# Kernel optimization log

Hardware: AMD Instinct MI355X
Metric: run time of the kernel (lower is better)

The kernel has to match this reference:

```python
import jax, jax.numpy as jnp
import numpy as np

D = 1024
H = 16
HEAD_DIM = D // H

def setup_inputs() -> dict:
    key = jax.random.key(0)
    ks = jax.random.split(key, 5)
    B, T = 2, 2048
    scale = 0.02
    x = jax.random.normal(ks[0], (B, T, D), dtype=jnp.float32)
    W_kqv = jax.random.normal(ks[1], (D, 3 * D), dtype=jnp.float32) * scale
    b_kqv = jnp.zeros((3 * D,), dtype=jnp.float32)
    W_proj = jax.random.normal(ks[2], (D, D), dtype=jnp.float32) * scale
    b_proj = jnp.zeros((D,), dtype=jnp.float32)
    return {"x": x, "W_kqv": W_kqv, "b_kqv": b_kqv, "W_proj": W_proj, "b_proj": b_proj}

def reference(x, W_kqv, b_kqv, W_proj, b_proj):
    B, T, d = x.shape
    qkv = x @ W_kqv + b_kqv  # [B,T,3d]
    q, k, v = jnp.split(qkv, 3, axis=-1)
    # [B, h, T, head_dim]
    def heads(t):
        return t.reshape(B, T, H, HEAD_DIM).transpose(0, 2, 1, 3)
    q, k, v = heads(q), heads(k), heads(v)
    scores = jnp.einsum("bhqd,bhkd->bhqk", q, k) / jnp.sqrt(jnp.float32(HEAD_DIM))
    causal = jnp.tril(jnp.ones((T, T), dtype=bool))  # True = keep
    scores = jnp.where(causal[None, None], scores, -jnp.inf)
    attn = jax.nn.softmax(scores, axis=-1)
    out = jnp.einsum("bhqk,bhkd->bhqd", attn, v)
    out = out.transpose(0, 2, 1, 3).reshape(B, T, d)
    return out @ W_proj + b_proj
```

## Files before the change

kernel.cpp:

```cpp
#include <hip/hip_runtime.h>
#include <hip/hip_bf16.h>
#include <cstdint>

typedef __bf16 bf16_t;
typedef __bf16 bf16x8 __attribute__((ext_vector_type(8)));
typedef __bf16 bf16x4 __attribute__((ext_vector_type(4)));
typedef float  f32x4  __attribute__((ext_vector_type(4)));

static constexpr int Bb = 2;
static constexpr int Tt = 2048;
static constexpr int Dd = 1024;
static constexpr int Hh = 16;
static constexpr int HD = 64;

#define QSCALE 0.18033688011112042f

__device__ __forceinline__ void async_copy16(const bf16_t* gsrc, bf16_t* ldst) {
    __builtin_amdgcn_global_load_lds(
        (const __attribute__((address_space(1))) unsigned int*)gsrc,
        (__attribute__((address_space(3))) unsigned int*)ldst, 16, 0, 0);
}

__global__ __launch_bounds__(256) void cvt_bf16_kernel(const float* __restrict__ in,
                                                       bf16_t* __restrict__ out, int n) {
    int i = (blockIdx.x * 256 + threadIdx.x) * 8;
    if (i >= n) return;
    float4 v0 = *(const float4*)(in + i);
    float4 v1 = *(const float4*)(in + i + 4);
    bf16x8 o;
    o[0] = (bf16_t)v0.x; o[1] = (bf16_t)v0.y; o[2] = (bf16_t)v0.z; o[3] = (bf16_t)v0.w;
    o[4] = (bf16_t)v1.x; o[5] = (bf16_t)v1.y; o[6] = (bf16_t)v1.z; o[7] = (bf16_t)v1.w;
    *(bf16x8*)(out + i) = o;
}

__global__ __launch_bounds__(256) void transpose_cvt(const float* __restrict__ in,
                                                     bf16_t* __restrict__ out,
                                                     int R, int C) {
    __shared__ bf16_t tile[64][72];
    int tr = blockIdx.y * 64, tc = blockIdx.x * 64;
    int t = threadIdx.x;
    int r = t >> 4;
    int c4 = (t & 15) * 4;
#pragma unroll
    for (int rr = 0; rr < 4; ++rr) {
        int row = r + rr * 16;
        float4 v = *(const float4*)(in + (size_t)(tr + row) * C + tc + c4);
        tile[c4 + 0][row] = (bf16_t)v.x;
        tile[c4 + 1][row] = (bf16_t)v.y;
        tile[c4 + 2][row] = (bf16_t)v.z;
        tile[c4 + 3][row] = (bf16_t)v.w;
    }
    __syncthreads();
#pragma unroll
    for (int rr = 0; rr < 4; ++rr) {
        int oc = r + rr * 16;
        bf16x4 o;
        o[0] = tile[oc][c4 + 0];
        o[1] = tile[oc][c4 + 1];
        o[2] = tile[oc][c4 + 2];
        o[3] = tile[oc][c4 + 3];
        *(bf16x4*)(out + (size_t)(tc + oc) * R + tr + c4) = o;
    }
}

template <int MODE, int NT>
__global__ __launch_bounds__(256) void gemm_bt(
    const bf16_t* __restrict__ A, const bf16_t* __restrict__ Bt,
    const float* __restrict__ bias, float* __restrict__ Cout,
    bf16_t* __restrict__ qb_, bf16_t* __restrict__ kb_, bf16_t* __restrict__ vb_,
    int M, int N, int K) {
    constexpr int NFRAG = NT / 32;
    __shared__ bf16_t As[128 * 64];
    __shared__ bf16_t Bs[NT * 64];
    int t = threadIdx.x;
    int wave = t >> 6, lane = t & 63;
    int l15 = lane & 15, quad = lane >> 4;
    int wm = wave & 1, wn = wave >> 1;
    int m0 = blockIdx.y * 128, n0 = blockIdx.x * NT;

    f32x4 acc[4][NFRAG];
#pragma unroll
    for (int mi = 0; mi < 4; ++mi)
#pragma unroll
        for (int ni = 0; ni < NFRAG; ++ni) acc[mi][ni] = (f32x4){0.f, 0.f, 0.f, 0.f};

    int kx = l15 & 7;

    for (int kk = 0; kk < K; kk += 64) {
        __syncthreads();
#pragma unroll
        for (int j = 0; j < 4; ++j) {
            int cid = j * 256 + t;
            int row = cid >> 3, sub = (cid & 7) ^ (row & 7);
            async_copy16(A + (size_t)(m0 + row) * K + kk + sub * 8, &As[cid * 8]);
        }
#pragma unroll
        for (int j = 0; j < NT / 32; ++j) {
            int cid = j * 256 + t;
            int row = cid >> 3, sub = (cid & 7) ^ (row & 7);
            async_copy16(Bt + (size_t)(n0 + row) * K + kk + sub * 8, &Bs[cid * 8]);
        }
        __syncthreads();
#pragma unroll
        for (int kb = 0; kb < 2; ++kb) {
            bf16x8 af[4], bf[NFRAG];
#pragma unroll
            for (int mi = 0; mi < 4; ++mi) {
                int r = wm * 64 + mi * 16 + l15;
                af[mi] = *(const bf16x8*)(&As[r * 64 + ((kb * 4 + quad) ^ kx) * 8]);
            }
#pragma unroll
            for (int ni = 0; ni < NFRAG; ++ni) {
                int r = wn * (NT / 2) + ni * 16 + l15;
                bf[ni] = *(const bf16x8*)(&Bs[r * 64 + ((kb * 4 + quad) ^ kx) * 8]);
            }
#pragma unroll
            for (int mi = 0; mi < 4; ++mi)
#pragma unroll
                for (int ni = 0; ni < NFRAG; ++ni)
                    acc[mi][ni] = __builtin_amdgcn_mfma_f32_16x16x32_bf16(af[mi], bf[ni], acc[mi][ni], 0, 0, 0);
        }
    }

    if (MODE == 1 && (n0 >> 10) == 2) {
#pragma unroll
        for (int ni = 0; ni < NFRAG; ++ni) {
            int col = n0 + wn * (NT / 2) + ni * 16 + l15;
            float bv = bias[col];
            int hh = (col >> 6) & 15, dd = col & 63;
#pragma unroll
            for (int mi = 0; mi < 4; ++mi) {
                int row = m0 + wm * 64 + mi * 16 + quad * 4;
                int bb = row >> 11, tt = row & (Tt - 1);
                bf16x4 pv;
#pragma unroll
                for (int r = 0; r < 4; ++r) pv[r] = (bf16_t)(acc[mi][ni][r] + bv);
                *(bf16x4*)(vb_ + ((size_t)(bb * Hh + hh) * HD + dd) * Tt + tt) = pv;
            }
        }
        return;
    }

#pragma unroll
    for (int ni = 0; ni < NFRAG; ++ni) {
        int col = n0 + wn * (NT / 2) + ni * 16 + l15;
        float bv = bias[col];
#pragma unroll
        for (int mi = 0; mi < 4; ++mi) {
#pragma unroll
            for (int r = 0; r < 4; ++r) {
                int row = m0 + wm * 64 + mi * 16 + quad * 4 + r;
                float v = acc[mi][ni][r] + bv;
                if (MODE == 0) {
                    Cout[(size_t)row * N + col] = v;
                } else {
                    int sec = col >> 10;
                    int hh = (col >> 6) & 15, dd = col & 63;
                    int bb = row >> 11, tt = row & (Tt - 1);
                    size_t idx = (((size_t)(bb * Hh + hh)) * Tt + tt) * HD + dd;
                    if (sec == 0) qb_[idx] = (bf16_t)(v * QSCALE);
                    else          kb_[idx] = (bf16_t)v;
                }
            }
        }
    }
}

__global__ __launch_bounds__(256, 4) void attn_kernel(
    const bf16_t* __restrict__ qb, const bf16_t* __restrict__ kb,
    const bf16_t* __restrict__ vb, bf16_t* __restrict__ ab) {
    __shared__ bf16_t Ks[64][72];
    __shared__ bf16_t Vs[64][72];
    __shared__ bf16_t Ps[4][16][72];
    int t = threadIdx.x;
    int wave = t >> 6, lane = t & 63;
    int l15 = lane & 15, quad = lane >> 4;
    int bh = blockIdx.y;
    int x = blockIdx.x;
    int qt = ((bh >> 3) & 1) ? (31 - x) : x;
    int b = bh >> 4, h = bh & 15;
    int qbase = qt * 64 + wave * 16;
    int q = qbase + l15;
    const bf16_t* qptr = qb + (size_t)bh * Tt * HD;
    const bf16_t* kptr = kb + (size_t)bh * Tt * HD;
    const bf16_t* vptr = vb + (size_t)bh * HD * Tt;

    bf16x8 qf[2];
    qf[0] = *(const bf16x8*)(qptr + (size_t)q * HD + quad * 8);
    qf[1] = *(const bf16x8*)(qptr + (size_t)q * HD + 32 + quad * 8);

    f32x4 o[4];
#pragma unroll
    for (int g = 0; g < 4; ++g) o[g] = (f32x4){0.f, 0.f, 0.f, 0.f};
    float mrow = -1e30f, lrow = 0.f;

    int srow = t >> 2;
    int scol = (t & 3) * 16;
    int qmax_w = qbase + 15;

    int nkt = qt + 1;
    for (int it = 0; it < nkt; ++it) {
        int kt0 = it * 64;
        __syncthreads();
        const bf16_t* kg = kptr + (size_t)(kt0 + srow) * HD + scol;
        *(bf16x8*)(&Ks[srow][scol])     = *(const bf16x8*)(kg);
        *(bf16x8*)(&Ks[srow][scol + 8]) = *(const bf16x8*)(kg + 8);
        const bf16_t* vg = vptr + (size_t)srow * Tt + kt0 + scol;
        *(bf16x8*)(&Vs[srow][scol])     = *(const bf16x8*)(vg);
        *(bf16x8*)(&Vs[srow][scol + 8]) = *(const bf16x8*)(vg + 8);
        __syncthreads();
        if (kt0 > qmax_w) continue;

        f32x4 s[4];
#pragma unroll
        for (int g = 0; g < 4; ++g) {
            s[g] = (f32x4){0.f, 0.f, 0.f, 0.f};
            bf16x8 kf0 = *(const bf16x8*)(&Ks[g * 16 + l15][quad * 8]);
            bf16x8 kf1 = *(const bf16x8*)(&Ks[g * 16 + l15][32 + quad * 8]);
            s[g] = __builtin_amdgcn_mfma_f32_16x16x32_bf16(kf0, qf[0], s[g], 0, 0, 0);
            s[g] = __builtin_amdgcn_mfma_f32_16x16x32_bf16(kf1, qf[1], s[g], 0, 0, 0);
        }

        if (kt0 + 63 > qbase) {
#pragma unroll
            for (int g = 0; g < 4; ++g)
#pragma unroll
                for (int r = 0; r < 4; ++r) {
                    int k_abs = kt0 + g * 16 + quad * 4 + r;
                    s[g][r] = (k_abs > q) ? -1e30f : s[g][r];
                }
        }

        float mloc = -1e30f;
#pragma unroll
        for (int g = 0; g < 4; ++g)
            mloc = fmaxf(mloc, fmaxf(fmaxf(s[g][0], s[g][1]), fmaxf(s[g][2], s[g][3])));
        mloc = fmaxf(mloc, __shfl_xor(mloc, 16));
        mloc = fmaxf(mloc, __shfl_xor(mloc, 32));
        float mnew = fmaxf(mrow, mloc);
        float alpha = exp2f(mrow - mnew);
        mrow = mnew;

        float rs = 0.f;
#pragma unroll
        for (int g = 0; g < 4; ++g) {
            float p0 = exp2f(s[g][0] - mnew);
            float p1 = exp2f(s[g][1] - mnew);
            float p2 = exp2f(s[g][2] - mnew);
            float p3 = exp2f(s[g][3] - mnew);
            rs += (p0 + p1) + (p2 + p3);
            bf16x4 pk;
            pk[0] = (bf16_t)p0; pk[1] = (bf16_t)p1; pk[2] = (bf16_t)p2; pk[3] = (bf16_t)p3;
            *(bf16x4*)(&Ps[wave][l15][g * 16 + quad * 4]) = pk;
        }
        rs += __shfl_xor(rs, 16);
        rs += __shfl_xor(rs, 32);
        lrow = lrow * alpha + rs;

#pragma unroll
        for (int g = 0; g < 4; ++g)
#pragma unroll
            for (int r = 0; r < 4; ++r) o[g][r] *= alpha;

#pragma unroll
        for (int kc = 0; kc < 2; ++kc) {
            bf16x8 pf = *(const bf16x8*)(&Ps[wave][l15][kc * 32 + quad * 8]);
#pragma unroll
            for (int g = 0; g < 4; ++g) {
                bf16x8 vf = *(const bf16x8*)(&Vs[g * 16 + l15][kc * 32 + quad * 8]);
                o[g] = __builtin_amdgcn_mfma_f32_16x16x32_bf16(vf, pf, o[g], 0, 0, 0);
            }
        }
    }

    float inv = 1.0f / lrow;
    size_t obase = ((size_t)b * Tt + q) * Dd + h * 64;
#pragma unroll
    for (int g = 0; g < 4; ++g) {
        bf16x4 ov;
#pragma unroll
        for (int r = 0; r < 4; ++r) ov[r] = (bf16_t)(o[g][r] * inv);
        *(bf16x4*)(ab + obase + g * 16 + quad * 4) = ov;
    }
}

extern "C" void kernel_launch(void* const* d_in, const int* in_sizes, int n_in,
                              void* d_out, int out_size, void* d_ws, size_t ws_size,
                              hipStream_t stream) {
    const float* x      = (const float*)d_in[0];
    const float* W_kqv  = (const float*)d_in[1];
    const float* b_kqv  = (const float*)d_in[2];
    const float* W_proj = (const float*)d_in[3];
    const float* b_proj = (const float*)d_in[4];
    float* out = (float*)d_out;
    char* ws = (char*)d_ws;
    const size_t MB = 1ull << 20;
    bf16_t* x_bf   = (bf16_t*)(ws + 0 * MB);
    bf16_t* wkqvt  = (bf16_t*)(ws + 8 * MB);
    bf16_t* wprojt = (bf16_t*)(ws + 14 * MB);
    bf16_t* qb     = (bf16_t*)(ws + 16 * MB);
    bf16_t* kb     = (bf16_t*)(ws + 24 * MB);
    bf16_t* vb     = (bf16_t*)(ws + 32 * MB);
    bf16_t* ab     = (bf16_t*)(ws + 40 * MB);

    cvt_bf16_kernel<<<(Bb * Tt * Dd) / (256 * 8), 256, 0, stream>>>(x, x_bf, Bb * Tt * Dd);
    transpose_cvt<<<dim3(3 * Dd / 64, Dd / 64), 256, 0, stream>>>(W_kqv, wkqvt, Dd, 3 * Dd);
    transpose_cvt<<<dim3(Dd / 64, Dd / 64), 256, 0, stream>>>(W_proj, wprojt, Dd, Dd);
    gemm_bt<1, 128><<<dim3(3 * Dd / 128, Bb * Tt / 128), 256, 0, stream>>>(
        x_bf, wkqvt, b_kqv, nullptr, qb, kb, vb, Bb * Tt, 3 * Dd, Dd);
    attn_kernel<<<dim3(32, Bb * Hh), 256, 0, stream>>>(qb, kb, vb, ab);
    gemm_bt<0, 64><<<dim3(Dd / 64, Bb * Tt / 128), 256, 0, stream>>>(
        ab, wprojt, b_proj, out, nullptr, nullptr, nullptr, Bb * Tt, Dd, Dd);
}
```

Measured before the change: 206.0 us.

## Fuse prep kernels into one launch and reorder attention grid heaviest-first

Merges the x conversion and both weight transpose-conversions into a single prep kernel that picks its job from the block index, removing two kernel launches and their gaps. Separately, the attention grid now puts batch*head on x and query tiles on y, reversed, so the longest causal tiles are dispatched first for all heads. This aims at better load balance at the tail of the causal attention kernel. The fused prep kernel carries shared-memory allocation even for the pure conversion blocks.

```diff
diff --git a/kernel.cpp b/kernel.cpp
--- a/kernel.cpp
+++ b/kernel.cpp
@@ -21,24 +21,35 @@
         (__attribute__((address_space(3))) unsigned int*)ldst, 16, 0, 0);
 }
 
-__global__ __launch_bounds__(256) void cvt_bf16_kernel(const float* __restrict__ in,
-                                                       bf16_t* __restrict__ out, int n) {
-    int i = (blockIdx.x * 256 + threadIdx.x) * 8;
-    if (i >= n) return;
-    float4 v0 = *(const float4*)(in + i);
-    float4 v1 = *(const float4*)(in + i + 4);
-    bf16x8 o;
-    o[0] = (bf16_t)v0.x; o[1] = (bf16_t)v0.y; o[2] = (bf16_t)v0.z; o[3] = (bf16_t)v0.w;
-    o[4] = (bf16_t)v1.x; o[5] = (bf16_t)v1.y; o[6] = (bf16_t)v1.z; o[7] = (bf16_t)v1.w;
-    *(bf16x8*)(out + i) = o;
-}
-
-__global__ __launch_bounds__(256) void transpose_cvt(const float* __restrict__ in,
-                                                     bf16_t* __restrict__ out,
-                                                     int R, int C) {
+__global__ __launch_bounds__(256) void prep_kernel(
+    const float* __restrict__ x, bf16_t* __restrict__ x_bf,
+    const float* __restrict__ Wk, bf16_t* __restrict__ wkqvt,
+    const float* __restrict__ Wp, bf16_t* __restrict__ wprojt) {
     __shared__ bf16_t tile[64][72];
-    int tr = blockIdx.y * 64, tc = blockIdx.x * 64;
+    int bid = blockIdx.x;
     int t = threadIdx.x;
+    if (bid < 2048) {
+        int i = (bid * 256 + t) * 8;
+        float4 v0 = *(const float4*)(x + i);
+        float4 v1 = *(const float4*)(x + i + 4);
+        bf16x8 o;
+        o[0] = (bf16_t)v0.x; o[1] = (bf16_t)v0.y; o[2] = (bf16_t)v0.z; o[3] = (bf16_t)v0.w;
+        o[4] = (bf16_t)v1.x; o[5] = (bf16_t)v1.y; o[6] = (bf16_t)v1.z; o[7] = (bf16_t)v1.w;
+        *(bf16x8*)(x_bf + i) = o;
+        return;
+    }
+    const float* in; bf16_t* out; int R, C, tr, tc;
+    if (bid < 2816) {
+        int id = bid - 2048;
+        R = Dd; C = 3 * Dd;
+        tc = (id % 48) * 64; tr = (id / 48) * 64;
+        in = Wk; out = wkqvt;
+    } else {
+        int id = bid - 2816;
+        R = Dd; C = Dd;
+        tc = (id & 15) * 64; tr = (id >> 4) * 64;
+        in = Wp; out = wprojt;
+    }
     int r = t >> 4;
     int c4 = (t & 15) * 4;
 #pragma unroll
@@ -175,9 +186,8 @@
     int t = threadIdx.x;
     int wave = t >> 6, lane = t & 63;
     int l15 = lane & 15, quad = lane >> 4;
-    int bh = blockIdx.y;
-    int x = blockIdx.x;
-    int qt = ((bh >> 3) & 1) ? (31 - x) : x;
+    int bh = blockIdx.x;
+    int qt = 31 - (int)blockIdx.y;
     int b = bh >> 4, h = bh & 15;
     int qbase = qt * 64 + wave * 16;
     int q = qbase + l15;
@@ -303,12 +313,10 @@
     bf16_t* vb     = (bf16_t*)(ws + 32 * MB);
     bf16_t* ab     = (bf16_t*)(ws + 40 * MB);
 
-    cvt_bf16_kernel<<<(Bb * Tt * Dd) / (256 * 8), 256, 0, stream>>>(x, x_bf, Bb * Tt * Dd);
-    transpose_cvt<<<dim3(3 * Dd / 64, Dd / 64), 256, 0, stream>>>(W_kqv, wkqvt, Dd, 3 * Dd);
-    transpose_cvt<<<dim3(Dd / 64, Dd / 64), 256, 0, stream>>>(W_proj, wprojt, Dd, Dd);
+    prep_kernel<<<3072, 256, 0, stream>>>(x, x_bf, W_kqv, wkqvt, W_proj, wprojt);
     gemm_bt<1, 128><<<dim3(3 * Dd / 128, Bb * Tt / 128), 256, 0, stream>>>(
         x_bf, wkqvt, b_kqv, nullptr, qb, kb, vb, Bb * Tt, 3 * Dd, Dd);
-    attn_kernel<<<dim3(32, Bb * Hh), 256, 0, stream>>>(qb, kb, vb, ab);
+    attn_kernel<<<dim3(Bb * Hh, 32), 256, 0, stream>>>(qb, kb, vb, ab);
     gemm_bt<0, 64><<<dim3(Dd / 64, Bb * Tt / 128), 256, 0, stream>>>(
         ab, wprojt, b_proj, out, nullptr, nullptr, nullptr, Bb * Tt, Dd, Dd);
 }
```

After: 194.2 us. 5.7% less time.
